# Optimization experiments

Measured on AMD Instinct MI355X. Metric: run time of the kernel, lower is better.

## Reference

```python
import jax, jax.numpy as jnp
import numpy as np

B, C, T, H, W, L = 4, 256, 8, 16, 16, 8
NO = 8                # num_offsets
D = C // NO           # per-head feature dim for offset/weight MLPs
EPS = 1e-5


def setup_inputs() -> dict:
    key = jax.random.key(0)
    ks = jax.random.split(key, 6)
    return {
        "features": jax.random.normal(ks[0], (B, C, T, H, W, L), jnp.float32),
        "pos": jax.random.normal(ks[1], (B, C, T, H, W, L), jnp.float32),
        "Wp": jax.random.normal(ks[2], (C, 3 * C), jnp.float32) * 0.02,  # 1x1x1 conv: 3C -> C
        "bp": jnp.zeros((C,), jnp.float32),
        "Wo": jax.random.normal(ks[3], (D, 3), jnp.float32) * 0.02,      # offset_embed Linear(d,3)
        "bo": jnp.zeros((3,), jnp.float32),
        "Ww": jax.random.normal(ks[4], (D, 2), jnp.float32) * 0.02,      # weight_embed Linear(d,2)
        "bw": jnp.zeros((2,), jnp.float32),
    }


def _trilinear_sample(feat, coords):
    """feat: (N,C,D1,D2,D3); coords: (N,G,3) in [-1,1] (axis order D1,D2,D3).
    align_corners=False, zeros padding (matches F.grid_sample semantics)."""
    N, Cc, D1, D2, D3 = feat.shape
    sizes = jnp.asarray([D1, D2, D3], feat.dtype)
    pix = ((coords + 1.0) * sizes - 1.0) * 0.5       # unnormalize to pixel coords
    lo = jnp.floor(pix)
    frac = pix - lo                                   # (N,G,3)
    lo = lo.astype(jnp.int32)
    dims = jnp.asarray([D1, D2, D3], jnp.int32)
    feat_flat = feat.reshape(N, Cc, D1 * D2 * D3)
    out = jnp.zeros((N, Cc, coords.shape[1]), feat.dtype)
    for dz in (0, 1):
        for dy in (0, 1):
            for dx in (0, 1):
                off = jnp.asarray([dz, dy, dx], jnp.int32)
                idx = lo + off                        # (N,G,3)
                wz = jnp.where(dz, frac[..., 0], 1.0 - frac[..., 0])
                wy = jnp.where(dy, frac[..., 1], 1.0 - frac[..., 1])
                wx = jnp.where(dx, frac[..., 2], 1.0 - frac[..., 2])
                wgt = wz * wy * wx                    # (N,G)
                valid = jnp.all((idx >= 0) & (idx < dims), axis=-1)
                idc = jnp.clip(idx, 0, dims - 1)
                lin = (idc[..., 0] * D2 + idc[..., 1]) * D3 + idc[..., 2]  # (N,G)
                vals = jnp.take_along_axis(feat_flat, lin[:, None, :], axis=2)  # (N,C,G)
                out = out + vals * (wgt * valid)[:, None, :]
    return out


def reference(features, pos, Wp, bp, Wo, bo, Ww, bw):
    Bv, Cv, Tv, Hv, Wv, Lv = features.shape
    BT = Bv * Tv
    feat = features.transpose(0, 2, 1, 3, 4, 5).reshape(BT, Cv, Hv, Wv, Lv)
    posr = pos.transpose(0, 2, 1, 3, 4, 5).reshape(BT, Cv, Hv, Wv, Lv)
    # global context + projection (1x1x1 conv over 3C channels) + ReLU
    glob = feat.mean(axis=(2, 3, 4), keepdims=True)
    src = jnp.concatenate([feat, posr, jnp.broadcast_to(glob, feat.shape)], axis=1)  # (BT,3C,H,W,L)
    proj = jax.nn.relu(jnp.einsum('nixyz,oi->noxyz', src, Wp) + bp[None, :, None, None, None])
    osrc = proj.transpose(0, 2, 3, 4, 1).reshape(BT, Hv, Wv, Lv, NO, D)
    # per-voxel per-head offsets in (0,1) and scalar weights
    offset = jax.nn.sigmoid(osrc @ Wo + bo)                      # (BT,H,W,L,NO,3)
    wgt = jax.nn.softmax(osrc @ Ww + bw, axis=-1)[..., 1]        # (BT,H,W,L,NO)
    # base flow field in [-1,1], deform in logit space, re-sigmoid
    base = jnp.stack(jnp.meshgrid(jnp.linspace(-1.0, 1.0, Hv),
                                  jnp.linspace(-1.0, 1.0, Wv),
                                  jnp.linspace(-1.0, 1.0, Lv), indexing='ij'), axis=-1)
    base01 = jnp.clip((base + 1.0) * 0.5, EPS, 1.0 - EPS)
    logit = jnp.log(base01 / (1.0 - base01))                     # (H,W,L,3)
    sp = jax.nn.sigmoid(logit[None, :, :, :, None, :] + offset)  # (BT,H,W,L,NO,3)
    grid = (sp * 2.0 - 1.0).transpose(0, 4, 1, 2, 3, 5).reshape(BT, NO * Hv * Wv * Lv, 3)
    sampled = _trilinear_sample(feat, grid).reshape(BT, Cv, NO, Hv, Wv, Lv)
    out = feat + jnp.einsum('bcnhwl,bhwln->bchwl', sampled, wgt)
    return out.reshape(Bv, Tv, Cv, Hv, Wv, Lv).transpose(0, 2, 1, 3, 4, 5)
```

## Files before the change

### kernel.cpp

```cpp
#include <hip/hip_runtime.h>

#define BB 4
#define CC 256
#define TT 8
#define HH 16
#define WW 16
#define LL 8
#define NO 8
#define DD 32
#define BT 32
#define VV 2048
#define KIN 512
#define EPS_ 1e-5f

typedef short bf16x8 __attribute__((ext_vector_type(8)));
typedef float f32x4 __attribute__((ext_vector_type(4)));
typedef float f32x2 __attribute__((ext_vector_type(2)));

static __device__ __forceinline__ float b2f(unsigned short u) {
    return __uint_as_float(((unsigned int)u) << 16);
}
static __device__ __forceinline__ float b2f_lo(unsigned int x) {
    return __uint_as_float(x << 16);
}
static __device__ __forceinline__ float b2f_hi(unsigned int x) {
    return __uint_as_float(x & 0xffff0000u);
}
static __device__ __forceinline__ unsigned short f2b(float f) {
    unsigned int x = __float_as_uint(f);
    unsigned int r = x + 0x7fffu + ((x >> 16) & 1u);
    return (unsigned short)(r >> 16);
}
static __device__ __forceinline__ unsigned int f2b_pk(float lo, float hi) {
    return (unsigned int)f2b(lo) | ((unsigned int)f2b(hi) << 16);
}
static __device__ __forceinline__ float sigm(float x) {
    return 1.0f / (1.0f + __expf(-x));
}

__global__ __launch_bounds__(256) void k0_prep(const float* __restrict__ Wp,
                                               unsigned short* __restrict__ Wa) {
    int i = blockIdx.x * 256 + threadIdx.x;
    int o = i >> 9, k = i & 511;
    Wa[i] = f2b(Wp[o * 768 + k]);
}

__global__ __launch_bounds__(256) void k1_transpose(const float* __restrict__ features,
                                                    const float* __restrict__ pos,
                                                    unsigned short* __restrict__ srcT) {
    const int n = blockIdx.x;
    const int vt = blockIdx.y;
    const int v0 = vt * 32;
    const int b = n >> 3, t = n & 7;
    const int tid = threadIdx.x;
    const int wv = tid >> 6;
    const int half = (tid >> 5) & 1;
    const int vl = tid & 31;

    __shared__ unsigned short sf[32 * 258];
    __shared__ unsigned short sp[32 * 258];

    const size_t base_ft = ((size_t)b * CC * TT + t) * (size_t)VV + v0 + vl;
    #pragma unroll 8
    for (int it = 0; it < 32; ++it) {
        const int c = it * 8 + wv * 2 + half;
        const size_t idx = base_ft + (size_t)c * (TT * VV);
        float f = features[idx];
        float p = pos[idx];
        sf[vl * 258 + c] = f2b(f);
        sp[vl * 258 + c] = f2b(p);
    }
    __syncthreads();

    unsigned int* srcU = (unsigned int*)srcT;
    const size_t obase = ((size_t)n * VV + v0) * 256;
    const int ku = tid;
    #pragma unroll 4
    for (int v = 0; v < 32; ++v) {
        unsigned int u;
        if (ku < 128) u = *(const unsigned int*)&sf[v * 258 + 2 * ku];
        else          u = *(const unsigned int*)&sp[v * 258 + 2 * (ku - 128)];
        srcU[obase + (size_t)v * 256 + ku] = u;
    }
}

__global__ __launch_bounds__(256) void k2a_gsum(const unsigned short* __restrict__ srcT,
                                                float* __restrict__ gpart) {
    const int n = blockIdx.x;
    const int vs = blockIdx.y;
    const int tid = threadIdx.x;
    const int ku = tid & 127;
    const int vh = tid >> 7;
    const unsigned int* srcU = (const unsigned int*)srcT;
    const size_t base = ((size_t)n * VV + vs * 128 + vh * 64) * 256 + ku;
    float sl = 0.f, sh = 0.f;
    #pragma unroll 8
    for (int i = 0; i < 64; ++i) {
        unsigned int u = srcU[base + (size_t)i * 256];
        sl += b2f_lo(u);
        sh += b2f_hi(u);
    }
    float2* gp = (float2*)gpart;
    gp[((size_t)n * 32 + vs * 2 + vh) * 128 + ku] = make_float2(sl, sh);
}

__global__ __launch_bounds__(256) void k2_gterm(const float* __restrict__ gpart,
                                                const float* __restrict__ Wp,
                                                const float* __restrict__ bp,
                                                float* __restrict__ gterm) {
    const int n = blockIdx.x;
    const int o = threadIdx.x;
    __shared__ float gl[CC];
    float s = 0.0f;
    const float* gp = gpart + (size_t)n * 32 * CC + o;
    #pragma unroll 8
    for (int vt = 0; vt < 32; ++vt) s += gp[vt * CC];
    gl[o] = s * (1.0f / (float)VV);
    __syncthreads();
    const float4* wrow = (const float4*)(Wp + (size_t)o * 768 + 512);
    const float4* g4 = (const float4*)gl;
    float acc = bp[o];
    #pragma unroll 8
    for (int c = 0; c < 64; ++c) {
        float4 w = wrow[c], g = g4[c];
        acc += w.x * g.x + w.y * g.y + w.z * g.z + w.w * g.w;
    }
    gterm[n * CC + o] = acc;
}

__global__ __launch_bounds__(256) void k3_gemm(const unsigned short* __restrict__ Wa,
                                               const unsigned short* __restrict__ srcT,
                                               const float* __restrict__ gterm,
                                               unsigned short* __restrict__ projT) {
    const int n  = blockIdx.x;
    const int mb = blockIdx.y;
    const int nb = blockIdx.z;
    const int tid = threadIdx.x;
    const int m0 = mb * 128, v0 = nb * 128;

    __shared__ short As[128 * 40];
    __shared__ short Bs[128 * 40];

    const int wv = tid >> 6;
    const int lane = tid & 63;
    const int wm = wv >> 1, wn = wv & 1;
    const int lr = lane & 15, lq = lane >> 4;

    f32x4 acc[4][4];
    #pragma unroll
    for (int i = 0; i < 4; ++i)
        #pragma unroll
        for (int j = 0; j < 4; ++j)
            acc[i][j] = (f32x4){0.f, 0.f, 0.f, 0.f};

    const int row = tid >> 1, half = tid & 1;
    const unsigned short* agp = Wa + (size_t)(m0 + row) * KIN + half * 16;
    const unsigned short* bgp = srcT + ((size_t)n * VV + v0 + row) * KIN + half * 16;
    short* asp = &As[row * 40 + half * 16];
    short* bsp = &Bs[row * 40 + half * 16];

    for (int k0 = 0; k0 < KIN; k0 += 32) {
        uint4 a0 = *(const uint4*)(agp + k0);
        uint4 a1 = *(const uint4*)(agp + k0 + 8);
        uint4 b0 = *(const uint4*)(bgp + k0);
        uint4 b1 = *(const uint4*)(bgp + k0 + 8);
        __syncthreads();
        *(uint4*)asp = a0; *(uint4*)(asp + 8) = a1;
        *(uint4*)bsp = b0; *(uint4*)(bsp + 8) = b1;
        __syncthreads();

        bf16x8 af[4], bf[4];
        #pragma unroll
        for (int i = 0; i < 4; ++i)
            af[i] = *(const bf16x8*)&As[(wm * 64 + i * 16 + lr) * 40 + lq * 8];
        #pragma unroll
        for (int j = 0; j < 4; ++j)
            bf[j] = *(const bf16x8*)&Bs[(wn * 64 + j * 16 + lr) * 40 + lq * 8];
        #pragma unroll
        for (int i = 0; i < 4; ++i)
            #pragma unroll
            for (int j = 0; j < 4; ++j)
                acc[i][j] = __builtin_amdgcn_mfma_f32_16x16x32_bf16(af[i], bf[j], acc[i][j], 0, 0, 0);
    }

    #pragma unroll
    for (int i = 0; i < 4; ++i) {
        const int og = m0 + wm * 64 + i * 16 + lq * 4;
        float4 g = *(const float4*)(gterm + n * CC + og);
        #pragma unroll
        for (int j = 0; j < 4; ++j) {
            const int vg = v0 + wn * 64 + j * 16 + lr;
            float x0 = fmaxf(acc[i][j][0] + g.x, 0.0f);
            float x1 = fmaxf(acc[i][j][1] + g.y, 0.0f);
            float x2 = fmaxf(acc[i][j][2] + g.z, 0.0f);
            float x3 = fmaxf(acc[i][j][3] + g.w, 0.0f);
            ushort4 st;
            st.x = f2b(x0); st.y = f2b(x1); st.z = f2b(x2); st.w = f2b(x3);
            *(ushort4*)&projT[((size_t)n * VV + vg) * CC + og] = st;
        }
    }
}

__global__ __launch_bounds__(256) void k4_coef(const unsigned short* __restrict__ projT,
                                               const float* __restrict__ Wo,
                                               const float* __restrict__ bo,
                                               const float* __restrict__ Ww,
                                               const float* __restrict__ bw,
                                               int2* __restrict__ pairs) {
    __shared__ float sWo[96], sWw[64], sb[5];
    const int tid = threadIdx.x;
    if (tid < 96) sWo[tid] = Wo[tid];
    if (tid < 64) sWw[tid] = Ww[tid];
    if (tid < 3)  sb[tid] = bo[tid];
    if (tid < 2)  sb[3 + tid] = bw[tid];
    __syncthreads();

    const int g = blockIdx.x * 256 + tid;
    const int n = g >> 14;
    const int rem = g & 16383;
    const int v = rem >> 3;
    const int hd = rem & 7;

    const uint4* up = (const uint4*)(projT + ((size_t)n * VV + v) * CC + hd * DD);
    float osrc[32];
    #pragma unroll
    for (int q = 0; q < 4; ++q) {
        uint4 u = up[q];
        unsigned int ws4[4] = {u.x, u.y, u.z, u.w};
        #pragma unroll
        for (int e = 0; e < 4; ++e) {
            osrc[q * 8 + e * 2]     = b2f_lo(ws4[e]);
            osrc[q * 8 + e * 2 + 1] = b2f_hi(ws4[e]);
        }
    }

    float o0 = sb[0], o1 = sb[1], o2 = sb[2];
    float zw = sb[4] - sb[3];
    #pragma unroll
    for (int d = 0; d < DD; ++d) {
        float t = osrc[d];
        o0 += t * sWo[3 * d + 0];
        o1 += t * sWo[3 * d + 1];
        o2 += t * sWo[3 * d + 2];
        zw += t * (sWw[2 * d + 1] - sWw[2 * d]);
    }
    const float wgt = sigm(zw);

    const int h = v >> 7, w = (v >> 3) & 15, l = v & 7;
    float ph = fminf(fmaxf(h * (1.0f / 15.0f), EPS_), 1.0f - EPS_);
    float pw = fminf(fmaxf(w * (1.0f / 15.0f), EPS_), 1.0f - EPS_);
    float pl = fminf(fmaxf(l * (1.0f / 7.0f),  EPS_), 1.0f - EPS_);
    float lh = __logf(ph / (1.0f - ph));
    float lw = __logf(pw / (1.0f - pw));
    float ll = __logf(pl / (1.0f - pl));

    float sph = sigm(lh + sigm(o0));
    float spw = sigm(lw + sigm(o1));
    float spl = sigm(ll + sigm(o2));
    float pixh = sph * 16.0f - 0.5f;
    float pixw = spw * 16.0f - 0.5f;
    float pixl = spl * 8.0f  - 0.5f;

    float flh = floorf(pixh), flw = floorf(pixw), fll = floorf(pixl);
    float fh = pixh - flh, fw = pixw - flw, fl = pixl - fll;
    int ih = (int)flh, iw = (int)flw, il = (int)fll;

    int2* pp = pairs + (size_t)g * 8;
    #pragma unroll
    for (int dz = 0; dz < 2; ++dz)
        #pragma unroll
        for (int dy = 0; dy < 2; ++dy)
            #pragma unroll
            for (int dx = 0; dx < 2; ++dx) {
                int iz = ih + dz, iy = iw + dy, ix = il + dx;
                float wt = (dz ? fh : 1.0f - fh) * (dy ? fw : 1.0f - fw) * (dx ? fl : 1.0f - fl) * wgt;
                bool valid = ((unsigned)iz < 16u) && ((unsigned)iy < 16u) && ((unsigned)ix < 8u);
                int lin = valid ? (((iz * 16 + iy) * 8 + ix) << 10) : 0;
                float wv2 = valid ? wt : 0.0f;
                pp[dz * 4 + dy * 2 + dx] = make_int2(lin, __float_as_int(wv2));
            }
}

__global__ __launch_bounds__(256) void k5_gather(const unsigned short* __restrict__ srcT,
                                                 const int2* __restrict__ pairs,
                                                 unsigned short* __restrict__ res) {
    __shared__ int2 pr[8 * 64];
    const int n  = blockIdx.x >> 8;
    const int vb = (blockIdx.x & 255) * 8;
    const int tid = threadIdx.x;

    {
        const int2* src = pairs + ((size_t)n * VV + vb) * 64;
        *(int4*)&pr[tid * 2] = *(const int4*)&src[tid * 2];
    }
    __syncthreads();

    const int s = tid >> 5;
    const int lane = tid & 31;
    const unsigned int laneoff = (unsigned int)lane * 16u;
    const char* slabB = (const char*)srcT + (size_t)n * VV * KIN * 2;
    const int2* pe = &pr[s * 64];

    f32x2 a0 = {0.f, 0.f}, a1 = {0.f, 0.f}, a2 = {0.f, 0.f}, a3 = {0.f, 0.f};

    #pragma unroll 1
    for (int e = 0; e < 64; e += 8) {
        uint4 f[8];
        float w[8];
        #pragma unroll
        for (int u = 0; u < 8; ++u) {
            int2 q = pe[e + u];
            w[u] = __int_as_float(q.y);
            f[u] = *(const uint4*)(slabB + ((unsigned int)q.x + laneoff));
        }
        #pragma unroll
        for (int u = 0; u < 8; ++u) {
            f32x2 w2 = {w[u], w[u]};
            f32x2 t0 = {b2f_lo(f[u].x), b2f_hi(f[u].x)};
            f32x2 t1 = {b2f_lo(f[u].y), b2f_hi(f[u].y)};
            f32x2 t2 = {b2f_lo(f[u].z), b2f_hi(f[u].z)};
            f32x2 t3 = {b2f_lo(f[u].w), b2f_hi(f[u].w)};
            a0 = __builtin_elementwise_fma(w2, t0, a0);
            a1 = __builtin_elementwise_fma(w2, t1, a1);
            a2 = __builtin_elementwise_fma(w2, t2, a2);
            a3 = __builtin_elementwise_fma(w2, t3, a3);
        }
    }

    uint4 st;
    st.x = f2b_pk(a0.x, a0.y);
    st.y = f2b_pk(a1.x, a1.y);
    st.z = f2b_pk(a2.x, a2.y);
    st.w = f2b_pk(a3.x, a3.y);
    *(uint4*)&res[((size_t)n * VV + vb + s) * CC + lane * 8] = st;
}

__global__ __launch_bounds__(256) void k6_final(const float* __restrict__ features,
                                                const unsigned short* __restrict__ res,
                                                float* __restrict__ out) {
    const int n = blockIdx.x;
    const int c0 = blockIdx.y * 64;
    const int v0 = blockIdx.z * 64;
    const int b = n >> 3, t = n & 7;
    const int tid = threadIdx.x;
    const int ty = tid >> 6, tx = tid & 63;

    __shared__ unsigned short t6[64 * 66];

    for (int vv = ty; vv < 64; vv += 4)
        t6[vv * 66 + tx] = res[((size_t)n * VV + v0 + vv) * CC + c0 + tx];
    __syncthreads();
    for (int cc = ty; cc < 64; cc += 4) {
        int c = c0 + cc;
        size_t oidx = (((size_t)b * CC + c) * TT + t) * VV + v0 + tx;
        out[oidx] = features[oidx] + b2f(t6[tx * 66 + cc]);
    }
}

extern "C" void kernel_launch(void* const* d_in, const int* in_sizes, int n_in,
                              void* d_out, int out_size, void* d_ws, size_t ws_size,
                              hipStream_t stream) {
    (void)in_sizes; (void)n_in; (void)out_size; (void)ws_size;
    const float* features = (const float*)d_in[0];
    const float* pos      = (const float*)d_in[1];
    const float* Wp       = (const float*)d_in[2];
    const float* bp       = (const float*)d_in[3];
    const float* Wo       = (const float*)d_in[4];
    const float* bo       = (const float*)d_in[5];
    const float* Ww       = (const float*)d_in[6];
    const float* bw       = (const float*)d_in[7];
    float* out = (float*)d_out;

    char* ws = (char*)d_ws;
    unsigned short* srcT  = (unsigned short*)ws;
    unsigned short* Wa    = (unsigned short*)(ws + 67108864);
    float*          gterm = (float*)(ws + 67403776);
    unsigned short* projT = (unsigned short*)(ws + 67436544);
    int2*           pairs = (int2*)(ws + 100990976);
    float*          gpart = (float*)(ws + 100990976);
    unsigned short* res   = projT;

    k0_prep<<<512, 256, 0, stream>>>(Wp, Wa);
    k1_transpose<<<dim3(32, 64), 256, 0, stream>>>(features, pos, srcT);
    k2a_gsum<<<dim3(32, 16), 256, 0, stream>>>(srcT, gpart);
    k2_gterm<<<32, 256, 0, stream>>>(gpart, Wp, bp, gterm);
    k3_gemm<<<dim3(32, 2, 16), 256, 0, stream>>>(Wa, srcT, gterm, projT);
    k4_coef<<<2048, 256, 0, stream>>>(projT, Wo, bo, Ww, bw, pairs);
    k5_gather<<<8192, 256, 0, stream>>>(srcT, pairs, res);
    k6_final<<<dim3(32, 4, 32), 256, 0, stream>>>(features, res, out);
}
```

Measured before the change: 371.5 us.

## Deduplicate gather corner indices per voxel with wave-level sort and segmented sum

Each voxel's 64 (index, weight) trilinear taps are sorted in-wave with a bitonic shuffle network. Weights for duplicate rows are combined with a segmented scan, and only the unique rows are gathered. Work moves from 8 voxels per block with 32 lanes × 8 channels to one voxel per wave with 64 lanes × 4 channels. The aim is fewer redundant global loads when neighbouring taps hit the same source voxel, at the cost of sort/scan shuffle overhead and narrower per-lane loads.

```diff
diff --git a/kernel.cpp b/kernel.cpp
--- a/kernel.cpp
+++ b/kernel.cpp
@@ -284,55 +284,75 @@
 __global__ __launch_bounds__(256) void k5_gather(const unsigned short* __restrict__ srcT,
                                                  const int2* __restrict__ pairs,
                                                  unsigned short* __restrict__ res) {
-    __shared__ int2 pr[8 * 64];
-    const int n  = blockIdx.x >> 8;
-    const int vb = (blockIdx.x & 255) * 8;
-    const int tid = threadIdx.x;
-
-    {
-        const int2* src = pairs + ((size_t)n * VV + vb) * 64;
-        *(int4*)&pr[tid * 2] = *(const int4*)&src[tid * 2];
-    }
-    __syncthreads();
-
-    const int s = tid >> 5;
-    const int lane = tid & 31;
-    const unsigned int laneoff = (unsigned int)lane * 16u;
-    const char* slabB = (const char*)srcT + (size_t)n * VV * KIN * 2;
-    const int2* pe = &pr[s * 64];
-
-    f32x2 a0 = {0.f, 0.f}, a1 = {0.f, 0.f}, a2 = {0.f, 0.f}, a3 = {0.f, 0.f};
-
+    __shared__ int   sK[4 * 64];
+    __shared__ float sW[4 * 64];
+    const int tid = threadIdx.x;
+    const int wid = tid >> 6;
+    const int lane = tid & 63;
+    const int gv = blockIdx.x * 4 + wid;
+    const int n = gv >> 11;
+    const int v = gv & 2047;
+
+    int2 q = pairs[(size_t)gv * 64 + lane];
+    int key = q.x;
+    float w = __int_as_float(q.y);
+
+    #pragma unroll
+    for (int k = 2; k <= 64; k <<= 1) {
+        #pragma unroll
+        for (int j = k >> 1; j > 0; j >>= 1) {
+            int pk = __shfl_xor(key, j);
+            float pw = __shfl_xor(w, j);
+            bool keepMin = (((lane & k) == 0) == ((lane & j) == 0));
+            bool take = keepMin ? (pk < key) : (pk > key);
+            if (take) { key = pk; w = pw; }
+        }
+    }
+    #pragma unroll
+    for (int d = 1; d < 64; d <<= 1) {
+        float tw = __shfl_up(w, d);
+        int   tk = __shfl_up(key, d);
+        if (lane >= d && tk == key) w += tw;
+    }
+    int nk = __shfl_down(key, 1);
+    bool tail = (lane == 63) || (nk != key);
+    unsigned long long mask = __ballot(tail);
+    int cnt = __popcll(mask);
+    int cidx = __popcll(mask & ((1ull << lane) - 1ull));
+
+    sK[wid * 64 + lane] = 0;
+    sW[wid * 64 + lane] = 0.0f;
+    __syncthreads();
+    if (tail) { sK[wid * 64 + cidx] = key; sW[wid * 64 + cidx] = w; }
+    __syncthreads();
+    int ck = sK[wid * 64 + lane];
+    float cw = sW[wid * 64 + lane];
+
+    const char* slabB = (const char*)srcT + (size_t)n * VV * KIN * 2 + lane * 8;
+    float a0 = 0.f, a1 = 0.f, a2 = 0.f, a3 = 0.f;
+    const int iters = (cnt + 7) & ~7;
     #pragma unroll 1
-    for (int e = 0; e < 64; e += 8) {
-        uint4 f[8];
-        float w[8];
+    for (int e = 0; e < iters; e += 8) {
+        uint2 f[8]; float wv[8];
         #pragma unroll
         for (int u = 0; u < 8; ++u) {
-            int2 q = pe[e + u];
-            w[u] = __int_as_float(q.y);
-            f[u] = *(const uint4*)(slabB + ((unsigned int)q.x + laneoff));
+            int rk = __shfl(ck, e + u);
+            wv[u] = __shfl(cw, e + u);
+            f[u] = *(const uint2*)(slabB + (unsigned)rk);
         }
         #pragma unroll
         for (int u = 0; u < 8; ++u) {
-            f32x2 w2 = {w[u], w[u]};
-            f32x2 t0 = {b2f_lo(f[u].x), b2f_hi(f[u].x)};
-            f32x2 t1 = {b2f_lo(f[u].y), b2f_hi(f[u].y)};
-            f32x2 t2 = {b2f_lo(f[u].z), b2f_hi(f[u].z)};
-            f32x2 t3 = {b2f_lo(f[u].w), b2f_hi(f[u].w)};
-            a0 = __builtin_elementwise_fma(w2, t0, a0);
-            a1 = __builtin_elementwise_fma(w2, t1, a1);
-            a2 = __builtin_elementwise_fma(w2, t2, a2);
-            a3 = __builtin_elementwise_fma(w2, t3, a3);
+            a0 = fmaf(wv[u], b2f_lo(f[u].x), a0);
+            a1 = fmaf(wv[u], b2f_hi(f[u].x), a1);
+            a2 = fmaf(wv[u], b2f_lo(f[u].y), a2);
+            a3 = fmaf(wv[u], b2f_hi(f[u].y), a3);
         }
     }
 
-    uint4 st;
-    st.x = f2b_pk(a0.x, a0.y);
-    st.y = f2b_pk(a1.x, a1.y);
-    st.z = f2b_pk(a2.x, a2.y);
-    st.w = f2b_pk(a3.x, a3.y);
-    *(uint4*)&res[((size_t)n * VV + vb + s) * CC + lane * 8] = st;
+    uint2 st;
+    st.x = f2b_pk(a0, a1);
+    st.y = f2b_pk(a2, a3);
+    *(uint2*)&res[((size_t)n * VV + v) * CC + lane * 4] = st;
 }
 
 __global__ __launch_bounds__(256) void k6_final(const float* __restrict__ features,
@@ -386,6 +406,6 @@
     k2_gterm<<<32, 256, 0, stream>>>(gpart, Wp, bp, gterm);
     k3_gemm<<<dim3(32, 2, 16), 256, 0, stream>>>(Wa, srcT, gterm, projT);
     k4_coef<<<2048, 256, 0, stream>>>(projT, Wo, bo, Ww, bw, pairs);
-    k5_gather<<<8192, 256, 0, stream>>>(srcT, pairs, res);
+    k5_gather<<<16384, 256, 0, stream>>>(srcT, pairs, res);
     k6_final<<<dim3(32, 4, 32), 256, 0, stream>>>(features, res, out);
 }
```

Result: faster. 349.3 us (-6.0%).
